# Optimization experiments

Hardware: AMD Instinct MI355X
Metric: run time of the kernel (lower is better)

The kernel has to match this reference:

```python
import jax, jax.numpy as jnp
import numpy as np

B, S, D, H, CS = 2, 4096, 1024, 16, 128
HD = D // H            # head_dim = 64
C = S // CS            # num_chunks = 32
NEG = -1e9


def setup_inputs() -> dict:
    key = jax.random.key(0)
    ks = jax.random.split(key, 13)
    w = lambda k: jax.random.normal(k, (D, D), jnp.float32) * 0.02
    b = lambda k: jax.random.normal(k, (D,), jnp.float32) * 0.02
    return {
        'hidden_states': jax.random.normal(ks[0], (B, S, D), jnp.float32),
        'Wq': w(ks[1]), 'bq': b(ks[2]),
        'Wk': w(ks[3]), 'bk': b(ks[4]),
        'Wv': w(ks[5]), 'bv': b(ks[6]),
        'Wo': w(ks[7]), 'bo': b(ks[8]),
        'Wr': w(ks[9]), 'br': b(ks[10]),
        'Wh': w(ks[11]), 'bh': b(ks[12]),
    }


def reference(hidden_states, Wq, bq, Wk, bk, Wv, bv, Wo, bo, Wr, br, Wh, bh):
    scale = 1.0 / np.sqrt(HD)
    proj = lambda x, W, bias: x @ W.T + bias  # torch nn.Linear convention

    # QKV, split heads: [B,H,C,CS,HD]
    def heads(x):
        return x.reshape(B, S, H, HD).transpose(0, 2, 1, 3).reshape(B, H, C, CS, HD)
    qc = heads(proj(hidden_states, Wq, bq))
    kc = heads(proj(hidden_states, Wk, bk))
    vc = heads(proj(hidden_states, Wv, bv))

    # Chunk representation = last token of each chunk (no padding since S % CS == 0)
    chunk_repr = hidden_states.reshape(B, C, CS, D)[:, :, -1, :]  # [B,C,D]
    r = proj(chunk_repr, Wr, br).reshape(B, C, H, HD).transpose(0, 2, 1, 3)  # [B,H,C,HD]
    h = proj(chunk_repr, Wh, bh).reshape(B, C, H, HD).transpose(0, 2, 1, 3)

    # Compressed chunk states F = K^T V per chunk: [B,H,C,HD,HD]
    f = jnp.einsum('bhcsd,bhcse->bhcde', kc, vc)

    # Inter-chunk retrieval (module uses triu mask: chunk i attends chunks j >= i)
    chunk_scores = jnp.einsum('bhcd,bhed->bhce', r, h) * scale  # [B,H,C,C]
    m_out = jnp.triu(jnp.ones((C, C), jnp.float32))
    chunk_scores = jnp.where(m_out == 0, NEG, chunk_scores)
    chunk_probs = jax.nn.softmax(chunk_scores, axis=-1)
    retrieved = jnp.einsum('bhce,bhexy->bhcxy', chunk_probs, f)  # [B,H,C,HD,HD]
    long_term = jnp.einsum('bhcsd,bhcde->bhcse', qc, retrieved)  # [B,H,C,CS,HD]

    # Intra-chunk attention, block-diagonal (mask is triu within chunk)
    local_scores = jnp.einsum('bhcsd,bhctd->bhcst', qc, kc) * scale  # [B,H,C,CS,CS]
    m_in = jnp.triu(jnp.ones((CS, CS), jnp.float32))
    local_scores = jnp.where(m_in == 0, NEG, local_scores)
    local_probs = jax.nn.softmax(local_scores, axis=-1)
    local_out = jnp.einsum('bhcst,bhctd->bhcsd', local_probs, vc)

    out = (long_term + local_out).reshape(B, H, S, HD).transpose(0, 2, 1, 3).reshape(B, S, D)
    return out @ Wo.T + bo
```

## Files before the change

### kernel.cpp

```cpp
#include <hip/hip_runtime.h>
#include <stdint.h>

#define NEG9 (-1e9f)

typedef __attribute__((ext_vector_type(8))) short short8;
typedef __attribute__((ext_vector_type(8))) unsigned short ushort8;
typedef __attribute__((ext_vector_type(4))) unsigned short ushort4_t;
typedef __attribute__((ext_vector_type(4))) float f32x4;

#define MFMA_BF16(a,b,c) __builtin_amdgcn_mfma_f32_16x16x32_bf16((a),(b),(c),0,0,0)

__device__ __forceinline__ unsigned short f2bf(float f) {
  union { float f; unsigned int u; } x; x.f = f;
  unsigned int r = x.u + 0x7fffu + ((x.u >> 16) & 1u);
  return (unsigned short)(r >> 16);
}
__device__ __forceinline__ float bf2f(unsigned short h) {
  union { unsigned int u; float f; } x; x.u = ((unsigned int)h) << 16;
  return x.f;
}
__device__ __forceinline__ void gload_lds16(const unsigned short* g, unsigned short* l) {
  __builtin_amdgcn_global_load_lds(
      (const __attribute__((address_space(1))) unsigned int*)g,
      (__attribute__((address_space(3))) unsigned int*)l, 16, 0, 0);
}

__global__ void cvt_f32_bf16(const float* __restrict__ in, unsigned short* __restrict__ out, int n4) {
  int i = blockIdx.x * blockDim.x + threadIdx.x;
  int stride = gridDim.x * blockDim.x;
  for (; i < n4; i += stride) {
    float4 v = ((const float4*)in)[i];
    ushort4_t o;
    o.x = f2bf(v.x); o.y = f2bf(v.y); o.z = f2bf(v.z); o.w = f2bf(v.w);
    ((ushort4_t*)out)[i] = o;
  }
}

__global__ void cvt_w6(const float* a0, const float* a1, const float* a2,
                       const float* a3, const float* a4, const float* a5,
                       unsigned short* b0, unsigned short* b1, unsigned short* b2,
                       unsigned short* b3, unsigned short* b4, unsigned short* b5) {
  const float* in; unsigned short* out;
  switch (blockIdx.y) {
    case 0: in = a0; out = b0; break;
    case 1: in = a1; out = b1; break;
    case 2: in = a2; out = b2; break;
    case 3: in = a3; out = b3; break;
    case 4: in = a4; out = b4; break;
    default: in = a5; out = b5; break;
  }
  const int n4 = 262144;
  int i = blockIdx.x * blockDim.x + threadIdx.x;
  int stride = gridDim.x * blockDim.x;
  for (; i < n4; i += stride) {
    float4 v = ((const float4*)in)[i];
    ushort4_t o;
    o.x = f2bf(v.x); o.y = f2bf(v.y); o.z = f2bf(v.z); o.w = f2bf(v.w);
    ((ushort4_t*)out)[i] = o;
  }
}

template<int OUT_F32>
__global__ __launch_bounds__(256)
void gemm_bt(const unsigned short* __restrict__ A,
             const unsigned short* __restrict__ W,
             const float* __restrict__ bias,
             void* __restrict__ Cout,
             int M, int N, int K) {
  __shared__ unsigned short As[128*32];
  __shared__ unsigned short Bs[128*32];
  const int t = threadIdx.x;
  const int lane = t & 63;
  const int wave = t >> 6;
  const int wr = wave >> 1, wc = wave & 1;
  const int lr = lane & 15;
  const int lk = (lane >> 4) << 3;

  const int nbn = N >> 7;
  const int nwg = (M >> 7) * nbn;
  int bid = blockIdx.x;
  if ((nwg & 7) == 0) { int q = nwg >> 3; bid = (bid & 7) * q + (bid >> 3); }
  const int bm = bid / nbn, bn = bid % nbn;

  const long rowA0 = (long)bm * 128;
  const long rowB0 = (long)bn * 128;
  const int srow = t >> 2;
  const int scol = (t & 3) << 3;

  f32x4 acc[4][4];
#pragma unroll
  for (int m = 0; m < 4; m++)
#pragma unroll
    for (int n = 0; n < 4; n++) acc[m][n] = f32x4{0.f,0.f,0.f,0.f};

  for (int k0 = 0; k0 < K; k0 += 32) {
    const unsigned short* ga = A + (rowA0 + srow) * K + k0 + scol;
    const unsigned short* gb = W + (rowB0 + srow) * K + k0 + scol;
    gload_lds16(ga,              As + t*8);
    gload_lds16(ga + (long)64*K, As + t*8 + 2048);
    gload_lds16(gb,              Bs + t*8);
    gload_lds16(gb + (long)64*K, Bs + t*8 + 2048);
    __syncthreads();
    short8 af[4], bf[4];
#pragma unroll
    for (int m = 0; m < 4; m++) af[m] = *(const short8*)&As[(wr*64 + m*16 + lr)*32 + lk];
#pragma unroll
    for (int n = 0; n < 4; n++) bf[n] = *(const short8*)&Bs[(wc*64 + n*16 + lr)*32 + lk];
#pragma unroll
    for (int m = 0; m < 4; m++)
#pragma unroll
      for (int n = 0; n < 4; n++)
        acc[m][n] = MFMA_BF16(af[m], bf[n], acc[m][n]);
    __syncthreads();
  }

  const int rg4 = (lane >> 4) * 4;
#pragma unroll
  for (int m = 0; m < 4; m++) {
#pragma unroll
    for (int n = 0; n < 4; n++) {
      long row = rowA0 + wr*64 + m*16 + rg4;
      long col = rowB0 + wc*64 + n*16 + lr;
      float bv = bias[col];
#pragma unroll
      for (int r = 0; r < 4; r++) {
        float v = acc[m][n][r] + bv;
        if (OUT_F32) ((float*)Cout)[(row + r) * N + col] = v;
        else ((unsigned short*)Cout)[(row + r) * N + col] = f2bf(v);
      }
    }
  }
}

__global__ __launch_bounds__(256)
void gemm_qkv(const unsigned short* __restrict__ A,
              const unsigned short* __restrict__ Wqkv,
              const float* __restrict__ bq, const float* __restrict__ bk,
              const float* __restrict__ bv,
              unsigned short* __restrict__ Q, unsigned short* __restrict__ Kb,
              unsigned short* __restrict__ V) {
  const int K = 1024;
  __shared__ unsigned short As[128*32];
  __shared__ unsigned short Bs[128*32];
  const int t = threadIdx.x;
  const int lane = t & 63;
  const int wave = t >> 6;
  const int wr = wave >> 1, wc = wave & 1;
  const int lr = lane & 15;
  const int lk = (lane >> 4) << 3;

  const int nbn = 24;
  int bid = blockIdx.x;
  { int q = 1536 >> 3; bid = (bid & 7) * q + (bid >> 3); }
  const int bm = bid / nbn, bn = bid % nbn;

  const long rowA0 = (long)bm * 128;
  const long rowB0 = (long)bn * 128;
  const int srow = t >> 2;
  const int scol = (t & 3) << 3;

  f32x4 acc[4][4];
#pragma unroll
  for (int m = 0; m < 4; m++)
#pragma unroll
    for (int n = 0; n < 4; n++) acc[m][n] = f32x4{0.f,0.f,0.f,0.f};

  for (int k0 = 0; k0 < K; k0 += 32) {
    const unsigned short* ga = A + (rowA0 + srow) * K + k0 + scol;
    const unsigned short* gb = Wqkv + (rowB0 + srow) * K + k0 + scol;
    gload_lds16(ga,              As + t*8);
    gload_lds16(ga + (long)64*K, As + t*8 + 2048);
    gload_lds16(gb,              Bs + t*8);
    gload_lds16(gb + (long)64*K, Bs + t*8 + 2048);
    __syncthreads();
    short8 af[4], bf[4];
#pragma unroll
    for (int m = 0; m < 4; m++) af[m] = *(const short8*)&As[(wr*64 + m*16 + lr)*32 + lk];
#pragma unroll
    for (int n = 0; n < 4; n++) bf[n] = *(const short8*)&Bs[(wc*64 + n*16 + lr)*32 + lk];
#pragma unroll
    for (int m = 0; m < 4; m++)
#pragma unroll
      for (int n = 0; n < 4; n++)
        acc[m][n] = MFMA_BF16(af[m], bf[n], acc[m][n]);
    __syncthreads();
  }

  const int which = bn >> 3;
  unsigned short* Co = (which == 0) ? Q : (which == 1) ? Kb : V;
  const float* bsel = (which == 0) ? bq : (which == 1) ? bk : bv;
  const long colbase = rowB0 - (long)which * 1024;

  const int rg4 = (lane >> 4) * 4;
#pragma unroll
  for (int m = 0; m < 4; m++) {
#pragma unroll
    for (int n = 0; n < 4; n++) {
      long row = rowA0 + wr*64 + m*16 + rg4;
      long col = colbase + wc*64 + n*16 + lr;
      float bvv = bsel[col];
#pragma unroll
      for (int r = 0; r < 4; r++)
        Co[(row + r) * 1024 + col] = f2bf(acc[m][n][r] + bvv);
    }
  }
}

__global__ void repr_pad(const float* __restrict__ hs, unsigned short* __restrict__ out,
                         const float* __restrict__ br, const float* __restrict__ bh,
                         float* __restrict__ brh) {
  int r = blockIdx.x;
  int t = threadIdx.x;
  long base = (long)r * 1024;
  if (r < 64) {
    int b = r >> 5, c = r & 31;
    const float* src = hs + ((long)(b*4096 + c*128 + 127)) * 1024;
#pragma unroll
    for (int j = 0; j < 4; j++) { int idx = t + j*256; out[base + idx] = f2bf(src[idx]); }
  } else {
#pragma unroll
    for (int j = 0; j < 4; j++) out[base + t + j*256] = 0;
    if (r == 64) {
#pragma unroll
      for (int j = 0; j < 4; j++) { int idx = t + j*256; brh[idx] = br[idx]; }
    } else if (r == 65) {
#pragma unroll
      for (int j = 0; j < 4; j++) { int idx = t + j*256; brh[1024 + idx] = bh[idx]; }
    }
  }
}

__global__ __launch_bounds__(1024) void chunk_probs_k(
    const unsigned short* __restrict__ rbh,
    float* __restrict__ probs) {
  __shared__ float rt[32][65];
  __shared__ float ht[32][65];
  int h = blockIdx.x, b = blockIdx.y;
  int t = threadIdx.x;
#pragma unroll
  for (int j = 0; j < 2; j++) {
    int idx = t + j*1024;
    int c = idx >> 6, d = idx & 63;
    rt[c][d] = bf2f(rbh[(long)(b*32 + c)*2048 + h*64 + d]);
    ht[c][d] = bf2f(rbh[(long)(b*32 + c)*2048 + 1024 + h*64 + d]);
  }
  __syncthreads();
  int e = t & 31, c = t >> 5;
  float s = 0.f;
#pragma unroll
  for (int d = 0; d < 64; d++) s += rt[c][d] * ht[e][d];
  s *= 0.125f;
  if (e < c) s = NEG9;
  float m = s;
#pragma unroll
  for (int off = 16; off > 0; off >>= 1) m = fmaxf(m, __shfl_xor(m, off, 32));
  float p = __expf(s - m);
  float sum = p;
#pragma unroll
  for (int off = 16; off > 0; off >>= 1) sum += __shfl_xor(sum, off, 32);
  probs[(((long)(b*16 + h))*32 + c)*32 + e] = p / sum;
}

__global__ __launch_bounds__(256) void f_kernel(
    const unsigned short* __restrict__ Kb, const unsigned short* __restrict__ Vb,
    unsigned short* __restrict__ f) {
  __shared__ unsigned short vT[64*136];
  __shared__ unsigned short kT[64*136];
  int bid = blockIdx.x;
  int c = bid & 31, h = (bid >> 5) & 15, b = bid >> 9;
  int t = threadIdx.x;
  const unsigned short* kg = Kb + ((long)(b*4096 + c*128))*1024 + h*64;
  const unsigned short* vg = Vb + ((long)(b*4096 + c*128))*1024 + h*64;
  {
    int eq = t & 7, sq = t >> 3;
    int s0 = sq*4, e0 = eq*8;
    ushort8 v[4], k[4];
#pragma unroll
    for (int r = 0; r < 4; r++) {
      v[r] = *(const ushort8*)&vg[(long)(s0 + r)*1024 + e0];
      k[r] = *(const ushort8*)&kg[(long)(s0 + r)*1024 + e0];
    }
#pragma unroll
    for (int x = 0; x < 8; x++) {
      ushort4_t pv, pk;
      pv.x = v[0][x]; pv.y = v[1][x]; pv.z = v[2][x]; pv.w = v[3][x];
      pk.x = k[0][x]; pk.y = k[1][x]; pk.z = k[2][x]; pk.w = k[3][x];
      *(ushort4_t*)&vT[(e0 + x)*136 + s0] = pv;
      *(ushort4_t*)&kT[(e0 + x)*136 + s0] = pk;
    }
  }
  __syncthreads();
  const int lane = t & 63, w = t >> 6;
  const int lr = lane & 15, lk = (lane >> 4) << 3;
  const int rg4 = (lane >> 4) * 4;
  const int e0w = (w & 1) * 32, d0w = (w >> 1) * 32;

  f32x4 acc[2][2];
#pragma unroll
  for (int m = 0; m < 2; m++)
#pragma unroll
    for (int n = 0; n < 2; n++) acc[m][n] = f32x4{0.f,0.f,0.f,0.f};
#pragma unroll
  for (int kk = 0; kk < 4; kk++) {
    short8 af[2], bf[2];
#pragma unroll
    for (int m = 0; m < 2; m++) af[m] = *(const short8*)&vT[(e0w + m*16 + lr)*136 + kk*32 + lk];
#pragma unroll
    for (int n = 0; n < 2; n++) bf[n] = *(const short8*)&kT[(d0w + n*16 + lr)*136 + kk*32 + lk];
#pragma unroll
    for (int m = 0; m < 2; m++)
#pragma unroll
      for (int n = 0; n < 2; n++) acc[m][n] = MFMA_BF16(af[m], bf[n], acc[m][n]);
  }
  unsigned short* fo = f + (long)bid * 4096;
#pragma unroll
  for (int m = 0; m < 2; m++)
#pragma unroll
    for (int n = 0; n < 2; n++)
#pragma unroll
      for (int r = 0; r < 4; r++)
        fo[(e0w + m*16 + rg4 + r)*64 + d0w + n*16 + lr] = f2bf(acc[m][n][r]);
}

__global__ __launch_bounds__(256) void retrieve_k(
    const float* __restrict__ probs, const unsigned short* __restrict__ f,
    unsigned short* __restrict__ retT) {
  __shared__ float PL[1024];
  int bh = blockIdx.x;
  int xt = blockIdx.y;
  int t = threadIdx.x;
  *(float4*)&PL[t*4] = *(const float4*)&probs[(long)bh*1024 + t*4];
  __syncthreads();
  const unsigned int* fb = (const unsigned int*)(f + (long)bh*32*4096);
  const int xo = xt*256 + t;
  unsigned int fv[32];
#pragma unroll
  for (int ec = 0; ec < 32; ec++) fv[ec] = fb[ec*2048 + xo];
  unsigned int* ro = (unsigned int*)retT + (long)bh*32*2048 + xo;
  for (int c = 0; c < 32; c++) {
    float a0 = 0.f, a1 = 0.f;
#pragma unroll
    for (int e4 = 0; e4 < 8; e4++) {
      float4 p = *(const float4*)&PL[c*32 + e4*4];
#pragma unroll
      for (int j = 0; j < 4; j++) {
        unsigned int v = fv[e4*4 + j];
        union { unsigned int u; float ff; } lo, hi;
        lo.u = v << 16; hi.u = v & 0xffff0000u;
        a0 += p[j] * lo.ff;
        a1 += p[j] * hi.ff;
      }
    }
    ro[(long)c*2048] = (unsigned int)f2bf(a0) | ((unsigned int)f2bf(a1) << 16);
  }
}

__global__ __launch_bounds__(256) void attn_k(
    const unsigned short* __restrict__ Qb,
    const unsigned short* __restrict__ Kb,
    const unsigned short* __restrict__ Vb,
    const unsigned short* __restrict__ retT,
    unsigned short* __restrict__ attn) {
  __shared__ unsigned short ks[128*64];
  __shared__ unsigned short vT[64*136];
  __shared__ unsigned short rT[64*64];
  __shared__ unsigned short P[128*136];
  const int bid = blockIdx.x;
  const int c = bid & 31, h = (bid >> 5) & 15, b = bid >> 9;
  const int t = threadIdx.x;
  const int lane = t & 63, w = t >> 6;
  const int lr = lane & 15, lk = (lane >> 4) << 3;
  const int rg4 = (lane >> 4) * 4;

  const long rowbase = (long)(b*4096 + c*128);
  const unsigned short* kg = Kb + rowbase*1024 + h*64;
  const unsigned short* vg = Vb + rowbase*1024 + h*64;
  const unsigned short* qg = Qb + rowbase*1024 + h*64;
  const unsigned short* rtg = retT + (long)bid*4096;

  {
    const int off = (t & 7) << 4;
#pragma unroll
    for (int i = 0; i < 4; i++) {
      int row = (t >> 3) + i*32;
      int srcoff = off ^ ((row & 7) << 4);
      gload_lds16(kg + (long)row*1024 + (srcoff >> 1), ks + t*8 + i*2048);
    }
#pragma unroll
    for (int i = 0; i < 2; i++) {
      int row = ((t + i*256) >> 3);
      int srcoff = off ^ ((row & 7) << 4);
      gload_lds16(rtg + (long)row*64 + (srcoff >> 1), rT + (t + i*256)*8);
    }
  }
  {
    int eq = t & 7, sq = t >> 3;
    int s0 = sq*4, e0 = eq*8;
    ushort8 v[4];
#pragma unroll
    for (int r = 0; r < 4; r++) v[r] = *(const ushort8*)&vg[(long)(s0 + r)*1024 + e0];
#pragma unroll
    for (int x = 0; x < 8; x++) {
      ushort4_t pv;
      pv.x = v[0][x]; pv.y = v[1][x]; pv.z = v[2][x]; pv.w = v[3][x];
      *(ushort4_t*)&vT[(e0 + x)*136 + s0] = pv;
    }
  }
  __syncthreads();

  short8 qa[2][2];
#pragma unroll
  for (int m = 0; m < 2; m++)
#pragma unroll
    for (int kk = 0; kk < 2; kk++)
      qa[m][kk] = *(const short8*)&qg[(long)(w*32 + m*16 + lr)*1024 + kk*32 + lk];
  f32x4 scf[2][8];
#pragma unroll
  for (int m = 0; m < 2; m++)
#pragma unroll
    for (int n = 0; n < 8; n++) scf[m][n] = f32x4{0.f,0.f,0.f,0.f};
#pragma unroll
  for (int n = 0; n < 8; n++) {
    const int krow = n*16 + lr;
    const int swzmask = (krow & 7) << 4;
#pragma unroll
    for (int kk = 0; kk < 2; kk++) {
      int colb = (kk*64 + ((lane >> 4) << 4)) ^ swzmask;
      short8 kf = *(const short8*)&ks[krow*64 + (colb >> 1)];
#pragma unroll
      for (int m = 0; m < 2; m++) scf[m][n] = MFMA_BF16(qa[m][kk], kf, scf[m][n]);
    }
  }

  float rsum[2][4];
#pragma unroll
  for (int m = 0; m < 2; m++) {
#pragma unroll
    for (int r = 0; r < 4; r++) {
      int srow = w*32 + m*16 + rg4 + r;
      float vals[8];
      float mx = -1e30f;
#pragma unroll
      for (int n = 0; n < 8; n++) {
        int tcol = n*16 + lr;
        float v_ = scf[m][n][r] * 0.125f;
        if (tcol < srow) v_ = NEG9;
        vals[n] = v_;
        mx = fmaxf(mx, v_);
      }
#pragma unroll
      for (int off = 1; off < 16; off <<= 1) mx = fmaxf(mx, __shfl_xor(mx, off, 16));
      float sum = 0.f;
#pragma unroll
      for (int n = 0; n < 8; n++) {
        float p = __expf(vals[n] - mx);
        sum += p;
        P[srow*136 + n*16 + lr] = f2bf(p);
      }
#pragma unroll
      for (int off = 1; off < 16; off <<= 1) sum += __shfl_xor(sum, off, 16);
      rsum[m][r] = sum;
    }
  }

  f32x4 outa[2][4];
#pragma unroll
  for (int m = 0; m < 2; m++)
#pragma unroll
    for (int n = 0; n < 4; n++) outa[m][n] = f32x4{0.f,0.f,0.f,0.f};
#pragma unroll
  for (int n = 0; n < 4; n++) {
    const int rrow = n*16 + lr;
    const int swzmask = (rrow & 7) << 4;
#pragma unroll
    for (int kk = 0; kk < 2; kk++) {
      int colb = (kk*64 + ((lane >> 4) << 4)) ^ swzmask;
      short8 rf = *(const short8*)&rT[rrow*64 + (colb >> 1)];
#pragma unroll
      for (int m = 0; m < 2; m++) outa[m][n] = MFMA_BF16(qa[m][kk], rf, outa[m][n]);
    }
  }

  f32x4 pv[2][4];
#pragma unroll
  for (int m = 0; m < 2; m++)
#pragma unroll
    for (int n = 0; n < 4; n++) pv[m][n] = f32x4{0.f,0.f,0.f,0.f};
#pragma unroll
  for (int kk = 0; kk < 4; kk++) {
    short8 pa[2];
#pragma unroll
    for (int m = 0; m < 2; m++) pa[m] = *(const short8*)&P[(w*32 + m*16 + lr)*136 + kk*32 + lk];
#pragma unroll
    for (int n = 0; n < 4; n++) {
      short8 vf = *(const short8*)&vT[(n*16 + lr)*136 + kk*32 + lk];
#pragma unroll
      for (int m = 0; m < 2; m++) pv[m][n] = MFMA_BF16(pa[m], vf, pv[m][n]);
    }
  }

  unsigned short* ao = attn + rowbase*1024 + h*64;
#pragma unroll
  for (int m = 0; m < 2; m++)
#pragma unroll
    for (int n = 0; n < 4; n++)
#pragma unroll
      for (int r = 0; r < 4; r++) {
        int srow = w*32 + m*16 + rg4 + r;
        float v_ = pv[m][n][r] / rsum[m][r] + outa[m][n][r];
        ao[(long)srow*1024 + n*16 + lr] = f2bf(v_);
      }
}

extern "C" void kernel_launch(void* const* d_in, const int* in_sizes, int n_in,
                              void* d_out, int out_size, void* d_ws, size_t ws_size,
                              hipStream_t stream) {
  const float* hs = (const float*)d_in[0];
  const float* Wq = (const float*)d_in[1];
  const float* bq = (const float*)d_in[2];
  const float* Wk = (const float*)d_in[3];
  const float* bk = (const float*)d_in[4];
  const float* Wv = (const float*)d_in[5];
  const float* bv = (const float*)d_in[6];
  const float* Wo = (const float*)d_in[7];
  const float* bo = (const float*)d_in[8];
  const float* Wr = (const float*)d_in[9];
  const float* br = (const float*)d_in[10];
  const float* Wh = (const float*)d_in[11];
  const float* bh = (const float*)d_in[12];

  char* p = (char*)d_ws;
  unsigned short* hsb  = (unsigned short*)p; p += (size_t)8192*1024*2;
  unsigned short* Wqkv = (unsigned short*)p; p += (size_t)3072*1024*2;
  unsigned short* Wob  = (unsigned short*)p; p += (size_t)1024*1024*2;
  unsigned short* Wrh  = (unsigned short*)p; p += (size_t)2048*1024*2;
  unsigned short* Qb   = (unsigned short*)p; p += (size_t)8192*1024*2;
  unsigned short* Kb   = (unsigned short*)p; p += (size_t)8192*1024*2;
  unsigned short* Vb   = (unsigned short*)p; p += (size_t)8192*1024*2;
  unsigned short* reprb= (unsigned short*)p; p += (size_t)128*1024*2;
  unsigned short* rbhb = (unsigned short*)p; p += (size_t)128*2048*2;
  float*          brh  = (float*)p;          p += (size_t)2048*4;
  float*          probs= (float*)p;          p += (size_t)2*16*32*32*4;
  unsigned short* fbuf = (unsigned short*)p; p += (size_t)2*16*32*4096*2;
  unsigned short* retT = (unsigned short*)p; p += (size_t)2*16*32*4096*2;
  unsigned short* attnb = hsb;

  cvt_f32_bf16<<<8192, 256, 0, stream>>>(hs, hsb, 2097152);
  cvt_w6<<<dim3(256, 6), 256, 0, stream>>>(Wq, Wk, Wv, Wo, Wr, Wh,
                                           Wqkv, Wqkv + (size_t)1024*1024,
                                           Wqkv + (size_t)2048*1024,
                                           Wob, Wrh, Wrh + (size_t)1024*1024);
  repr_pad<<<128, 256, 0, stream>>>(hs, reprb, br, bh, brh);

  gemm_qkv<<<1536, 256, 0, stream>>>(hsb, Wqkv, bq, bk, bv, Qb, Kb, Vb);

  gemm_bt<0><<<16, 256, 0, stream>>>(reprb, Wrh, brh, rbhb, 128, 2048, 1024);

  chunk_probs_k<<<dim3(16, 2), 1024, 0, stream>>>(rbhb, probs);

  f_kernel<<<1024, 256, 0, stream>>>(Kb, Vb, fbuf);

  retrieve_k<<<dim3(32, 8), 256, 0, stream>>>(probs, fbuf, retT);

  attn_k<<<1024, 256, 0, stream>>>(Qb, Kb, Vb, retT, attnb);

  gemm_bt<1><<<512, 256, 0, stream>>>(attnb, Wob, bo, d_out, 8192, 1024, 1024);
}
```

Before: 293.2 us.

## Replace QKV and output GEMMs with 256x256-tile double-buffered 8-wave kernel

```diff
diff --git a/kernel.cpp b/kernel.cpp
--- a/kernel.cpp
+++ b/kernel.cpp
@@ -57,6 +57,189 @@
     ushort4_t o;
     o.x = f2bf(v.x); o.y = f2bf(v.y); o.z = f2bf(v.z); o.w = f2bf(v.w);
     ((ushort4_t*)out)[i] = o;
+  }
+}
+
+__device__ __forceinline__ void stage_half(const unsigned short* __restrict__ g, int ldg,
+                                           unsigned short* lh, int t) {
+#pragma unroll
+  for (int j = 0; j < 2; j++) {
+    int idx = j*512 + t;
+    int rowh = idx >> 3;
+    int colb = (idx & 7) << 4;
+    int scol = colb ^ ((rowh & 7) << 4);
+    gload_lds16(g + (long)rowh*ldg + (scol >> 1), lh + idx*8);
+  }
+}
+
+template<int MODE>
+__global__ __launch_bounds__(512, 2)
+void gemm8(const unsigned short* __restrict__ A,
+           const unsigned short* __restrict__ W,
+           const float* __restrict__ b0, const float* __restrict__ b1,
+           const float* __restrict__ b2,
+           void* __restrict__ o0, void* __restrict__ o1, void* __restrict__ o2,
+           int M, int N, int K) {
+  __shared__ unsigned short lds[2][2][16384];
+  const int t = threadIdx.x;
+  const int lane = t & 63;
+  const int w = t >> 6;
+  const int wm = w >> 2, wn = w & 3;
+  const int lr = lane & 15, lp = lane >> 4;
+
+  const int nbn = N >> 8;
+  const int nwg = (M >> 8) * nbn;
+  int bid = blockIdx.x;
+  { int q = nwg >> 3; bid = (bid & 7) * q + (bid >> 3); }
+  const int bm = bid / nbn, bn = bid % nbn;
+  const long rowA0 = (long)bm << 8;
+  const long rowB0 = (long)bn << 8;
+  const int KT = K >> 6;
+
+  stage_half(W + rowB0*K,         K, &lds[0][1][0],    t);
+  stage_half(W + (rowB0+128)*K,   K, &lds[0][1][8192], t);
+  stage_half(A + rowA0*K,         K, &lds[0][0][0],    t);
+  stage_half(A + (rowA0+128)*K,   K, &lds[0][0][8192], t);
+  if (KT > 1) {
+    stage_half(W + rowB0*K + 64,       K, &lds[1][1][0],    t);
+    stage_half(W + (rowB0+128)*K + 64, K, &lds[1][1][8192], t);
+  }
+  asm volatile("s_waitcnt vmcnt(4)" ::: "memory");
+  __builtin_amdgcn_s_barrier();
+
+  f32x4 acc[8][4];
+#pragma unroll
+  for (int m = 0; m < 8; m++)
+#pragma unroll
+    for (int n = 0; n < 4; n++) acc[m][n] = f32x4{0.f,0.f,0.f,0.f};
+
+  short8 af[4][2], bf0[2][2], bf1[2][2];
+
+  for (int kt = 0; kt < KT; ++kt) {
+    const int cur = kt & 1;
+    const char* As = (const char*)&lds[cur][0][0];
+    const char* Bs = (const char*)&lds[cur][1][0];
+
+#pragma unroll
+    for (int mr = 0; mr < 4; mr++) {
+      int row = wm*128 + mr*16 + lr;
+      int sw = (row & 7) << 4;
+#pragma unroll
+      for (int kk = 0; kk < 2; kk++)
+        af[mr][kk] = *(const short8*)(As + row*128 + ((kk*64 + lp*16) ^ sw));
+    }
+#pragma unroll
+    for (int nr = 0; nr < 2; nr++) {
+      int row = wn*64 + nr*16 + lr;
+      int sw = (row & 7) << 4;
+#pragma unroll
+      for (int kk = 0; kk < 2; kk++)
+        bf0[nr][kk] = *(const short8*)(Bs + row*128 + ((kk*64 + lp*16) ^ sw));
+    }
+    if (kt+1 < KT) stage_half(A + rowA0*K + (kt+1)*64, K, &lds[cur^1][0][0], t);
+    __builtin_amdgcn_s_barrier();
+    __builtin_amdgcn_s_setprio(1);
+#pragma unroll
+    for (int mr = 0; mr < 4; mr++)
+#pragma unroll
+      for (int nr = 0; nr < 2; nr++)
+#pragma unroll
+        for (int kk = 0; kk < 2; kk++)
+          acc[mr][nr] = MFMA_BF16(af[mr][kk], bf0[nr][kk], acc[mr][nr]);
+    __builtin_amdgcn_s_setprio(0);
+    __builtin_amdgcn_s_barrier();
+
+#pragma unroll
+    for (int nr = 0; nr < 2; nr++) {
+      int row = wn*64 + 32 + nr*16 + lr;
+      int sw = (row & 7) << 4;
+#pragma unroll
+      for (int kk = 0; kk < 2; kk++)
+        bf1[nr][kk] = *(const short8*)(Bs + row*128 + ((kk*64 + lp*16) ^ sw));
+    }
+    if (kt+1 < KT) stage_half(A + (rowA0+128)*K + (kt+1)*64, K, &lds[cur^1][0][8192], t);
+    __builtin_amdgcn_s_barrier();
+    __builtin_amdgcn_s_setprio(1);
+#pragma unroll
+    for (int mr = 0; mr < 4; mr++)
+#pragma unroll
+      for (int nr = 0; nr < 2; nr++)
+#pragma unroll
+        for (int kk = 0; kk < 2; kk++)
+          acc[mr][2+nr] = MFMA_BF16(af[mr][kk], bf1[nr][kk], acc[mr][2+nr]);
+    __builtin_amdgcn_s_setprio(0);
+    __builtin_amdgcn_s_barrier();
+
+#pragma unroll
+    for (int mr = 0; mr < 4; mr++) {
+      int row = wm*128 + 64 + mr*16 + lr;
+      int sw = (row & 7) << 4;
+#pragma unroll
+      for (int kk = 0; kk < 2; kk++)
+        af[mr][kk] = *(const short8*)(As + row*128 + ((kk*64 + lp*16) ^ sw));
+    }
+    if (kt+2 < KT) stage_half(W + rowB0*K + (kt+2)*64, K, &lds[cur][1][0], t);
+    __builtin_amdgcn_s_barrier();
+    __builtin_amdgcn_s_setprio(1);
+#pragma unroll
+    for (int mr = 0; mr < 4; mr++)
+#pragma unroll
+      for (int nr = 0; nr < 2; nr++)
+#pragma unroll
+        for (int kk = 0; kk < 2; kk++)
+          acc[4+mr][2+nr] = MFMA_BF16(af[mr][kk], bf1[nr][kk], acc[4+mr][2+nr]);
+    __builtin_amdgcn_s_setprio(0);
+    __builtin_amdgcn_s_barrier();
+
+    if (kt+2 < KT) stage_half(W + (rowB0+128)*K + (kt+2)*64, K, &lds[cur][1][8192], t);
+    __builtin_amdgcn_s_barrier();
+    __builtin_amdgcn_s_setprio(1);
+#pragma unroll
+    for (int mr = 0; mr < 4; mr++)
+#pragma unroll
+      for (int nr = 0; nr < 2; nr++)
+#pragma unroll
+        for (int kk = 0; kk < 2; kk++)
+          acc[4+mr][nr] = MFMA_BF16(af[mr][kk], bf0[nr][kk], acc[4+mr][nr]);
+    __builtin_amdgcn_s_setprio(0);
+    if (kt+1 < KT) {
+      if (kt+2 < KT) { asm volatile("s_waitcnt vmcnt(4)" ::: "memory"); }
+      else           { asm volatile("s_waitcnt vmcnt(0)" ::: "memory"); }
+    }
+    __builtin_amdgcn_s_barrier();
+  }
+
+  if (MODE == 2) {
+    const int which = (int)(rowB0 >> 10);
+    unsigned short* Co = which==0 ? (unsigned short*)o0 : which==1 ? (unsigned short*)o1 : (unsigned short*)o2;
+    const float* bb = which==0 ? b0 : which==1 ? b1 : b2;
+    const long colbase = rowB0 - (long)which*1024;
+#pragma unroll
+    for (int m = 0; m < 8; m++)
+#pragma unroll
+      for (int n = 0; n < 4; n++) {
+        long row = rowA0 + wm*128 + m*16 + lp*4;
+        long col = colbase + wn*64 + n*16 + lr;
+        float bv = bb[col];
+#pragma unroll
+        for (int r = 0; r < 4; r++)
+          Co[(row + r)*1024 + col] = f2bf(acc[m][n][r] + bv);
+      }
+  } else {
+#pragma unroll
+    for (int m = 0; m < 8; m++)
+#pragma unroll
+      for (int n = 0; n < 4; n++) {
+        long row = rowA0 + wm*128 + m*16 + lp*4;
+        long col = rowB0 + wn*64 + n*16 + lr;
+        float bv = b0[col];
+#pragma unroll
+        for (int r = 0; r < 4; r++) {
+          float v = acc[m][n][r] + bv;
+          if (MODE == 1) ((float*)o0)[(row + r)*N + col] = v;
+          else ((unsigned short*)o0)[(row + r)*N + col] = f2bf(v);
+        }
+      }
   }
 }
 
@@ -128,80 +311,6 @@
         if (OUT_F32) ((float*)Cout)[(row + r) * N + col] = v;
         else ((unsigned short*)Cout)[(row + r) * N + col] = f2bf(v);
       }
-    }
-  }
-}
-
-__global__ __launch_bounds__(256)
-void gemm_qkv(const unsigned short* __restrict__ A,
-              const unsigned short* __restrict__ Wqkv,
-              const float* __restrict__ bq, const float* __restrict__ bk,
-              const float* __restrict__ bv,
-              unsigned short* __restrict__ Q, unsigned short* __restrict__ Kb,
-              unsigned short* __restrict__ V) {
-  const int K = 1024;
-  __shared__ unsigned short As[128*32];
-  __shared__ unsigned short Bs[128*32];
-  const int t = threadIdx.x;
-  const int lane = t & 63;
-  const int wave = t >> 6;
-  const int wr = wave >> 1, wc = wave & 1;
-  const int lr = lane & 15;
-  const int lk = (lane >> 4) << 3;
-
-  const int nbn = 24;
-  int bid = blockIdx.x;
-  { int q = 1536 >> 3; bid = (bid & 7) * q + (bid >> 3); }
-  const int bm = bid / nbn, bn = bid % nbn;
-
-  const long rowA0 = (long)bm * 128;
-  const long rowB0 = (long)bn * 128;
-  const int srow = t >> 2;
-  const int scol = (t & 3) << 3;
-
-  f32x4 acc[4][4];
-#pragma unroll
-  for (int m = 0; m < 4; m++)
-#pragma unroll
-    for (int n = 0; n < 4; n++) acc[m][n] = f32x4{0.f,0.f,0.f,0.f};
-
-  for (int k0 = 0; k0 < K; k0 += 32) {
-    const unsigned short* ga = A + (rowA0 + srow) * K + k0 + scol;
-    const unsigned short* gb = Wqkv + (rowB0 + srow) * K + k0 + scol;
-    gload_lds16(ga,              As + t*8);
-    gload_lds16(ga + (long)64*K, As + t*8 + 2048);
-    gload_lds16(gb,              Bs + t*8);
-    gload_lds16(gb + (long)64*K, Bs + t*8 + 2048);
-    __syncthreads();
-    short8 af[4], bf[4];
-#pragma unroll
-    for (int m = 0; m < 4; m++) af[m] = *(const short8*)&As[(wr*64 + m*16 + lr)*32 + lk];
-#pragma unroll
-    for (int n = 0; n < 4; n++) bf[n] = *(const short8*)&Bs[(wc*64 + n*16 + lr)*32 + lk];
-#pragma unroll
-    for (int m = 0; m < 4; m++)
-#pragma unroll
-      for (int n = 0; n < 4; n++)
-        acc[m][n] = MFMA_BF16(af[m], bf[n], acc[m][n]);
-    __syncthreads();
-  }
-
-  const int which = bn >> 3;
-  unsigned short* Co = (which == 0) ? Q : (which == 1) ? Kb : V;
-  const float* bsel = (which == 0) ? bq : (which == 1) ? bk : bv;
-  const long colbase = rowB0 - (long)which * 1024;
-
-  const int rg4 = (lane >> 4) * 4;
-#pragma unroll
-  for (int m = 0; m < 4; m++) {
-#pragma unroll
-    for (int n = 0; n < 4; n++) {
-      long row = rowA0 + wr*64 + m*16 + rg4;
-      long col = colbase + wc*64 + n*16 + lr;
-      float bvv = bsel[col];
-#pragma unroll
-      for (int r = 0; r < 4; r++)
-        Co[(row + r) * 1024 + col] = f2bf(acc[m][n][r] + bvv);
     }
   }
 }
@@ -552,17 +661,15 @@
                                            Wob, Wrh, Wrh + (size_t)1024*1024);
   repr_pad<<<128, 256, 0, stream>>>(hs, reprb, br, bh, brh);
 
-  gemm_qkv<<<1536, 256, 0, stream>>>(hsb, Wqkv, bq, bk, bv, Qb, Kb, Vb);
+  gemm8<2><<<384, 512, 0, stream>>>(hsb, Wqkv, bq, bk, bv, Qb, Kb, Vb, 8192, 3072, 1024);
 
   gemm_bt<0><<<16, 256, 0, stream>>>(reprb, Wrh, brh, rbhb, 128, 2048, 1024);
 
   chunk_probs_k<<<dim3(16, 2), 1024, 0, stream>>>(rbhb, probs);
-
   f_kernel<<<1024, 256, 0, stream>>>(Kb, Vb, fbuf);
-
   retrieve_k<<<dim3(32, 8), 256, 0, stream>>>(probs, fbuf, retT);
-
   attn_k<<<1024, 256, 0, stream>>>(Qb, Kb, Vb, retT, attnb);
 
-  gemm_bt<1><<<512, 256, 0, stream>>>(attnb, Wob, bo, d_out, 8192, 1024, 1024);
-}
+  gemm8<1><<<128, 512, 0, stream>>>(attnb, Wob, bo, nullptr, nullptr,
+                                    d_out, nullptr, nullptr, 8192, 1024, 1024);
+}
```

Measured after the change: 289.8 us. No clear change (-1.2%).
